# Optimization experiments

Measured on AMD Instinct MI355X. Metric: run time of the kernel, lower is better.

The kernel has to match this reference:

```python
import jax, jax.numpy as jnp
import numpy as np

Z_DIM = 16
N_EVAL = 1
MAX_LATENT_VARIANCE = 0.1


def _decoder(z, V1, c1, V2, c2, Vsig, csig):
    # z: (B, n) -> x_star: (B, D), sigma: (B,) per-sample positive scalar
    h = jnp.tanh(z @ V1 + c1)
    x_star = h @ V2 + c2
    sigma = jax.nn.softplus(h @ Vsig + csig)[:, 0] + 1e-3
    return x_star, sigma


def _encoder(x, W1, b1, W2, b2):
    h = jnp.tanh(x @ W1 + b1)
    return h @ W2 + b2


def _f_hess(z, x, dec):
    # faithful port of function_for_hessian: scalar per-sample energy
    D = x.shape[0]
    x_star, sigma = _decoder(z[None], *dec)
    d = (x[None] - x_star) / sigma[:, None]
    return (d * d).sum() / 2 + D * jnp.log(sigma).sum() + (z ** 2).sum() / 2


def setup_inputs() -> dict:
    key = jax.random.key(0)
    ks = jax.random.split(key, 8)
    B, D, H, n = 256, 3072, 2048, Z_DIM
    return {
        "x": jax.random.uniform(ks[0], (B, D), jnp.float32),
        "W1": jax.random.normal(ks[1], (D, H), jnp.float32) / np.sqrt(D).astype(np.float32),
        "b1": jnp.zeros((H,), jnp.float32),
        "W2": jax.random.normal(ks[2], (H, n), jnp.float32) / np.sqrt(H).astype(np.float32),
        "b2": jnp.zeros((n,), jnp.float32),
        "V1": jax.random.normal(ks[3], (n, H), jnp.float32) / np.sqrt(n).astype(np.float32),
        "c1": jnp.zeros((H,), jnp.float32),
        "V2": jax.random.normal(ks[4], (H, D), jnp.float32) / np.sqrt(H).astype(np.float32),
        "c2": jnp.zeros((D,), jnp.float32),
        "Vsig": jax.random.normal(ks[5], (H, 1), jnp.float32) / np.sqrt(H).astype(np.float32),
        "csig": jnp.zeros((1,), jnp.float32),
        "eps": jax.random.normal(ks[6], (N_EVAL, B, n), jnp.float32),
    }


def reference(x, W1, b1, W2, b2, V1, c1, V2, c2, Vsig, csig, eps):
    dec = (V1, c1, V2, c2, Vsig, csig)
    z_star = _encoder(x, W1, b1, W2, b2)            # (B, n)
    B, D = x.shape
    n = z_star.shape[1]
    n_eval = eps.shape[0]

    # per-sample Hessian of the energy wrt z (double autodiff through decoder)
    hess = jax.vmap(jax.hessian(_f_hess), in_axes=(0, 0, None))(z_star, x, dec)  # (B, n, n)

    eigvals = jnp.linalg.eigvalsh(hess)             # (B, n)
    delta = jnp.maximum(1.0 / MAX_LATENT_VARIANCE - eigvals.min(axis=1), 0.0)    # (B,)
    Prec = hess + jnp.eye(n, dtype=hess.dtype) * delta[:, None, None]
    eigvals = eigvals + delta[:, None]

    # upper Cholesky U with U^T U = Prec (matches torch cholesky(upper=True))
    U = jnp.swapaxes(jnp.linalg.cholesky(Prec), -1, -2)
    sol = jax.vmap(lambda e: jax.lax.linalg.triangular_solve(
        U, e[..., None], left_side=True, lower=False)[..., 0])(eps)  # (n_eval, B, n)
    z_sample = z_star[None] + sol

    recon, sigma = _decoder(z_sample.reshape(-1, n), *dec)           # (n_eval*B, D), (n_eval*B,)
    x_rep = jnp.tile(x, (n_eval, 1))
    recon_loss = (((recon - x_rep) / sigma[:, None]) ** 2).sum(axis=1) / 2
    recon_loss = recon_loss.reshape(n_eval, B).mean(axis=0)

    latent_energy = (z_star ** 2).sum(axis=1) / 2 + (1.0 / eigvals).sum(axis=1) / 2
    logdet_loss = jnp.log(eigvals).sum(axis=1) / 2
    sigma_loss = (D * jnp.log(sigma)).reshape(n_eval, B).mean(axis=0)

    neg_log_prob = (recon_loss + latent_energy + logdet_loss + sigma_loss) / D
    return neg_log_prob
```

## Files before the change

kernel.cpp:

```cpp
#include <hip/hip_runtime.h>
#include <math.h>

#define B_N 256
#define D_N 3072
#define H_N 2048

typedef __bf16 bf16x8 __attribute__((ext_vector_type(8)));
typedef float f32x4 __attribute__((ext_vector_type(4)));

__device__ __forceinline__ void async16(const void* g, void* l) {
  __builtin_amdgcn_global_load_lds(
      (const __attribute__((address_space(1))) unsigned int*)g,
      (__attribute__((address_space(3))) unsigned int*)l, 16, 0, 0);
}

template<int EPI>
__global__ __launch_bounds__(256) void gemm_nn(const float* __restrict__ A,
        const float* __restrict__ Bm, const float* __restrict__ bias,
        const float* __restrict__ X, float* __restrict__ C,
        int M, int N, int K) {
  __shared__ __align__(16) float As[16][64];
  __shared__ __align__(16) float Bs[16][68];
  int tid = threadIdx.x;
  int tx = tid & 15, ty = tid >> 4;
  int n0 = blockIdx.x * 64, m0 = blockIdx.y * 64;
  float acc[4][4] = {};
  int am = tid >> 2, akq = (tid & 3) * 4;
  int bn = tid & 63, bk0 = (tid >> 6) * 4;
  for (int k0 = 0; k0 < K; k0 += 16) {
    float4 a4 = *(const float4*)(A + (size_t)(m0 + am) * K + k0 + akq);
    As[akq + 0][am] = a4.x; As[akq + 1][am] = a4.y;
    As[akq + 2][am] = a4.z; As[akq + 3][am] = a4.w;
#pragma unroll
    for (int p = 0; p < 4; ++p) {
      int kk = bk0 + p;
      Bs[kk][bn] = Bm[(size_t)(k0 + kk) * N + n0 + bn];
    }
    __syncthreads();
#pragma unroll
    for (int kk = 0; kk < 16; ++kk) {
      float4 av = *(const float4*)&As[kk][ty * 4];
      float4 bv = *(const float4*)&Bs[kk][tx * 4];
      float a_[4] = {av.x, av.y, av.z, av.w};
      float b_[4] = {bv.x, bv.y, bv.z, bv.w};
#pragma unroll
      for (int i = 0; i < 4; ++i)
#pragma unroll
        for (int j = 0; j < 4; ++j)
          acc[i][j] = fmaf(a_[i], b_[j], acc[i][j]);
    }
    __syncthreads();
  }
#pragma unroll
  for (int i = 0; i < 4; ++i) {
    int m = m0 + ty * 4 + i;
#pragma unroll
    for (int j = 0; j < 4; ++j) {
      int n = n0 + tx * 4 + j;
      float v = acc[i][j];
      if (EPI == 0) {
        v = tanhf(v + bias[n]);
      } else {
        v = X[(size_t)m * N + n] - v - bias[n];
      }
      C[(size_t)m * N + n] = v;
    }
  }
}

__global__ __launch_bounds__(256) void gemm_nt(const float* __restrict__ A,
        const float* __restrict__ B2, float* __restrict__ C, int M, int N, int K) {
  __shared__ __align__(16) float As[16][64];
  __shared__ __align__(16) float Bs[16][68];
  int tid = threadIdx.x;
  int tx = tid & 15, ty = tid >> 4;
  int n0 = blockIdx.x * 64, m0 = blockIdx.y * 64;
  float acc[4][4] = {};
  int am = tid >> 2, akq = (tid & 3) * 4;
  for (int k0 = 0; k0 < K; k0 += 16) {
    float4 a4 = *(const float4*)(A + (size_t)(m0 + am) * K + k0 + akq);
    As[akq + 0][am] = a4.x; As[akq + 1][am] = a4.y;
    As[akq + 2][am] = a4.z; As[akq + 3][am] = a4.w;
    float4 b4 = *(const float4*)(B2 + (size_t)(n0 + am) * K + k0 + akq);
    Bs[akq + 0][am] = b4.x; Bs[akq + 1][am] = b4.y;
    Bs[akq + 2][am] = b4.z; Bs[akq + 3][am] = b4.w;
    __syncthreads();
#pragma unroll
    for (int kk = 0; kk < 16; ++kk) {
      float4 av = *(const float4*)&As[kk][ty * 4];
      float4 bv = *(const float4*)&Bs[kk][tx * 4];
      float a_[4] = {av.x, av.y, av.z, av.w};
      float b_[4] = {bv.x, bv.y, bv.z, bv.w};
#pragma unroll
      for (int i = 0; i < 4; ++i)
#pragma unroll
        for (int j = 0; j < 4; ++j)
          acc[i][j] = fmaf(a_[i], b_[j], acc[i][j]);
    }
    __syncthreads();
  }
#pragma unroll
  for (int i = 0; i < 4; ++i)
#pragma unroll
    for (int j = 0; j < 4; ++j)
      C[(size_t)(m0 + ty * 4 + i) * N + n0 + tx * 4 + j] = acc[i][j];
}

template<int EPI>
__global__ __launch_bounds__(256) void mfma_gemm(const float* __restrict__ A,
        const __bf16* __restrict__ Bt, const float* __restrict__ bias,
        const float* __restrict__ X, float* __restrict__ C,
        int M, int N, int K) {
  __shared__ __align__(16) __bf16 Aa[64][72];
  __shared__ __align__(16) __bf16 Bb[64][72];
  int tid = threadIdx.x;
  int lane = tid & 63, w = tid >> 6;
  int n0 = blockIdx.x * 64, m0 = blockIdx.y * 64;
  f32x4 acc[4] = {};
  int srow = tid >> 2, sk = (tid & 3) * 16;
  const float* arow_p = A + (size_t)(m0 + srow) * K;
  const __bf16* brow_p = Bt + (size_t)(n0 + srow) * K;
  int ar = lane & 15, aq = (lane >> 4) * 8;
  for (int k0 = 0; k0 < K; k0 += 64) {
    __bf16 tmp[16];
#pragma unroll
    for (int p = 0; p < 16; p += 4) {
      float4 a4 = *(const float4*)(arow_p + k0 + sk + p);
      tmp[p + 0] = (__bf16)a4.x; tmp[p + 1] = (__bf16)a4.y;
      tmp[p + 2] = (__bf16)a4.z; tmp[p + 3] = (__bf16)a4.w;
    }
    *(uint4*)&Aa[srow][sk] = *(uint4*)&tmp[0];
    *(uint4*)&Aa[srow][sk + 8] = *(uint4*)&tmp[8];
    *(uint4*)&Bb[srow][sk] = *(const uint4*)(brow_p + k0 + sk);
    *(uint4*)&Bb[srow][sk + 8] = *(const uint4*)(brow_p + k0 + sk + 8);
    __syncthreads();
#pragma unroll
    for (int kk = 0; kk < 64; kk += 32) {
      bf16x8 a = *(const bf16x8*)&Aa[w * 16 + ar][kk + aq];
#pragma unroll
      for (int cg = 0; cg < 4; ++cg) {
        bf16x8 bb = *(const bf16x8*)&Bb[cg * 16 + ar][kk + aq];
        acc[cg] = __builtin_amdgcn_mfma_f32_16x16x32_bf16(a, bb, acc[cg], 0, 0, 0);
      }
    }
    __syncthreads();
  }
  int crow = (lane >> 4) * 4;
#pragma unroll
  for (int cg = 0; cg < 4; ++cg) {
#pragma unroll
    for (int r = 0; r < 4; ++r) {
      int m = m0 + w * 16 + crow + r;
      int n = n0 + cg * 16 + ar;
      float v = acc[cg][r];
      if (EPI == 0) v = tanhf(v + bias[n]);
      else if (EPI == 1) v = X[(size_t)m * N + n] - v - bias[n];
      C[(size_t)m * N + n] = v;
    }
  }
}

__global__ __launch_bounds__(256) void gemm64_sk(const __bf16* __restrict__ A,
        const __bf16* __restrict__ Bt, float* __restrict__ P, int M, int N, int K) {
  __shared__ __align__(16) __bf16 Ab[64 * 64];
  __shared__ __align__(16) __bf16 Bb[64 * 64];
  int tid = threadIdx.x;
  int lane = tid & 63, w = tid >> 6;
  int n0 = blockIdx.x * 64, m0 = blockIdx.y * 64;
  int k0 = blockIdx.z * 512;
  int srow = lane >> 3;
  int schunk = (lane & 7) ^ (srow & 7);
  const char* gA[2];
  const char* gB[2];
#pragma unroll
  for (int i = 0; i < 2; ++i) {
    int r = 16 * w + 8 * i + srow;
    gA[i] = (const char*)(A + (size_t)(m0 + r) * K + k0) + schunk * 16;
    gB[i] = (const char*)(Bt + (size_t)(n0 + r) * K + k0) + schunk * 16;
  }
  f32x4 acc[4] = {};
  int ar = lane & 15, aq = (lane >> 4) * 8;
  int sw = ar & 7;
  for (int it = 0; it < 8; ++it) {
#pragma unroll
    for (int i = 0; i < 2; ++i) {
      async16(gA[i], (char*)Ab + (16 * w + 8 * i) * 128);
      async16(gB[i], (char*)Bb + (16 * w + 8 * i) * 128);
      gA[i] += 128;
      gB[i] += 128;
    }
    __syncthreads();
#pragma unroll
    for (int kk = 0; kk < 64; kk += 32) {
      int ch = (kk + aq) >> 3;
      int coff = (ch ^ sw) * 16;
      bf16x8 a = *(const bf16x8*)((char*)Ab + (16 * w + ar) * 128 + coff);
#pragma unroll
      for (int cg = 0; cg < 4; ++cg) {
        bf16x8 bb = *(const bf16x8*)((char*)Bb + (cg * 16 + ar) * 128 + coff);
        acc[cg] = __builtin_amdgcn_mfma_f32_16x16x32_bf16(a, bb, acc[cg], 0, 0, 0);
      }
    }
    __syncthreads();
  }
  int q = lane >> 4;
  float* Pz = P + (size_t)blockIdx.z * M * N;
#pragma unroll
  for (int cg = 0; cg < 4; ++cg)
#pragma unroll
    for (int r = 0; r < 4; ++r) {
      int m = m0 + 16 * w + q * 4 + r;
      int n = n0 + cg * 16 + ar;
      Pz[(size_t)m * N + n] = acc[cg][r];
    }
}

template<int EPI, int WBF>
__global__ __launch_bounds__(256) void reduce_epi(const float* __restrict__ P,
        const float* __restrict__ bias, const float* __restrict__ X,
        float* __restrict__ C, __bf16* __restrict__ Cbf, int M, int N, int S) {
  int idx = (blockIdx.x * 256 + threadIdx.x) * 4;
  size_t MN = (size_t)M * N;
  float4 s = *(const float4*)(P + idx);
  for (int z = 1; z < S; ++z) {
    float4 p = *(const float4*)(P + z * MN + idx);
    s.x += p.x; s.y += p.y; s.z += p.z; s.w += p.w;
  }
  int n = idx % N;
  float v[4] = {s.x, s.y, s.z, s.w};
  if (EPI == 0) {
#pragma unroll
    for (int j = 0; j < 4; ++j) v[j] = tanhf(v[j] + bias[n + j]);
  } else if (EPI == 1) {
    float4 xv = *(const float4*)(X + idx);
    float xa[4] = {xv.x, xv.y, xv.z, xv.w};
#pragma unroll
    for (int j = 0; j < 4; ++j) v[j] = xa[j] - v[j] - bias[n + j];
  }
  *(float4*)(C + idx) = make_float4(v[0], v[1], v[2], v[3]);
  if (WBF) {
    __bf16 t[4] = {(__bf16)v[0], (__bf16)v[1], (__bf16)v[2], (__bf16)v[3]};
    *(uint2*)(Cbf + idx) = *(uint2*)&t[0];
  }
}

__global__ __launch_bounds__(256) void build_J(const float* __restrict__ h,
        const float* __restrict__ V1, __bf16* __restrict__ J) {
  int row = blockIdx.x;
  int b = row >> 4, i = row & 15;
  int k = threadIdx.x * 8;
  const float* hp = h + (size_t)b * H_N + k;
  const float* vp = V1 + (size_t)i * H_N + k;
  float4 h0 = *(const float4*)hp, h1 = *(const float4*)(hp + 4);
  float4 v0 = *(const float4*)vp, v1 = *(const float4*)(vp + 4);
  __bf16 t[8];
  t[0] = (__bf16)((1.f - h0.x * h0.x) * v0.x);
  t[1] = (__bf16)((1.f - h0.y * h0.y) * v0.y);
  t[2] = (__bf16)((1.f - h0.z * h0.z) * v0.z);
  t[3] = (__bf16)((1.f - h0.w * h0.w) * v0.w);
  t[4] = (__bf16)((1.f - h1.x * h1.x) * v1.x);
  t[5] = (__bf16)((1.f - h1.y * h1.y) * v1.y);
  t[6] = (__bf16)((1.f - h1.z * h1.z) * v1.z);
  t[7] = (__bf16)((1.f - h1.w * h1.w) * v1.w);
  *(uint4*)(J + (size_t)row * H_N + k) = *(uint4*)&t[0];
}

__global__ __launch_bounds__(256) void gemm128_nt_bf16(
        const __bf16* __restrict__ A, const __bf16* __restrict__ B,
        __bf16* __restrict__ C, int M, int N, int K) {
  __shared__ __align__(16) __bf16 Ab[128 * 64];
  __shared__ __align__(16) __bf16 Bb[128 * 64];
  int tid = threadIdx.x;
  int lane = tid & 63, w = tid >> 6;
  int m0 = blockIdx.y * 128, n0 = blockIdx.x * 128;
  int wm = w & 1, wn = w >> 1;
// ... 23 lines not shown
    for (int kk = 0; kk < 64; kk += 32) {
      int ch = (kk + aq) >> 3;
      int coff = (ch ^ sw) * 16;
      bf16x8 af[4], bfr[4];
#pragma unroll
      for (int f = 0; f < 4; ++f) {
        int rowA = wm * 64 + f * 16 + ar;
        af[f] = *(const bf16x8*)((char*)Ab + rowA * 128 + coff);
        int rowB = wn * 64 + f * 16 + ar;
        bfr[f] = *(const bf16x8*)((char*)Bb + rowB * 128 + coff);
      }
#pragma unroll
      for (int i = 0; i < 4; ++i)
#pragma unroll
        for (int j = 0; j < 4; ++j)
          acc[i][j] = __builtin_amdgcn_mfma_f32_16x16x32_bf16(af[i], bfr[j],
                                                              acc[i][j], 0, 0, 0);
    }
    __syncthreads();
  }
  int q = lane >> 4;
#pragma unroll
  for (int i = 0; i < 4; ++i)
#pragma unroll
    for (int j = 0; j < 4; ++j)
#pragma unroll
      for (int r = 0; r < 4; ++r) {
        int m = m0 + wm * 64 + i * 16 + q * 4 + r;
        int n = n0 + wn * 64 + j * 16 + ar;
        C[(size_t)m * N + n] = (__bf16)acc[i][j][r];
      }
}

__global__ __launch_bounds__(256) void gram16(const __bf16* __restrict__ Mbf,
        const float* __restrict__ coef, float* __restrict__ Hm) {
  __shared__ float red[4][16][17];
  int b = blockIdx.x;
  int tid = threadIdx.x, lane = tid & 63, w = tid >> 6;
  int ar = lane & 15, q = lane >> 4;
  const __bf16* row = Mbf + (size_t)(b * 16 + ar) * D_N + w * (D_N / 4);
  f32x4 acc = {};
  for (int k = 0; k < D_N / 4; k += 32) {
    bf16x8 a = *(const bf16x8*)(row + k + q * 8);
    acc = __builtin_amdgcn_mfma_f32_16x16x32_bf16(a, a, acc, 0, 0, 0);
  }
#pragma unroll
  for (int r = 0; r < 4; ++r) red[w][q * 4 + r][ar] = acc[r];
  __syncthreads();
  int i = tid >> 4, j = tid & 15;
  float g = red[0][i][j] + red[1][i][j] + red[2][i][j] + red[3][i][j];
  Hm[(size_t)b * 256 + tid] += coef[b * 4] * g;
}

__global__ __launch_bounds__(256) void small_mfma3(const float* __restrict__ h,
        const float* __restrict__ t, const float* __restrict__ Vsig,
        const float* __restrict__ V1, const float* __restrict__ coef,
        float* __restrict__ Hm) {
  __shared__ float redT[4][16][17];
  __shared__ float redP[4][4][16];
  __shared__ float redQ[4][4][16];
  int b = blockIdx.x;
  int tid = threadIdx.x, lane = tid & 63, w = tid >> 6;
  int m = lane & 15, q = lane >> 4;
  float a1 = coef[b * 4 + 0], a2 = coef[b * 4 + 1];
  float beta = coef[b * 4 + 2], csp = coef[b * 4 + 3];
  const float* hb = h + (size_t)b * H_N;
  const float* tb = t + (size_t)b * H_N;
  const float* vr = V1 + (size_t)m * H_N;
  f32x4 accT = {};
  float pacc = 0.f, qacc = 0.f;
  for (int s = 0; s < 16; ++s) {
    int kb = w * 512 + s * 32 + q * 8;
    float hv[8], tv[8], sv[8], v1v[8];
    *(float4*)&hv[0] = *(const float4*)(hb + kb);
    *(float4*)&hv[4] = *(const float4*)(hb + kb + 4);
    *(float4*)&tv[0] = *(const float4*)(tb + kb);
    *(float4*)&tv[4] = *(const float4*)(tb + kb + 4);
    *(float4*)&sv[0] = *(const float4*)(Vsig + kb);
    *(float4*)&sv[4] = *(const float4*)(Vsig + kb + 4);
    *(float4*)&v1v[0] = *(const float4*)(vr + kb);
    *(float4*)&v1v[4] = *(const float4*)(vr + kb + 4);
    __bf16 ah[8], al[8], bh[8], bl[8];
#pragma unroll
    for (int j = 0; j < 8; ++j) {
      float hk = hv[j];
      float dk = 1.f - hk * hk;
      float g = fmaf(csp, sv[j], -a1 * tv[j]);
      float wk = -2.f * g * hk * dk;
      float av = wk * v1v[j];
      __bf16 avh = (__bf16)av;
      ah[j] = avh;
      al[j] = (__bf16)(av - (float)avh);
      __bf16 bvh = (__bf16)v1v[j];
      bh[j] = bvh;
      bl[j] = (__bf16)(v1v[j] - (float)bvh);
      pacc = fmaf(dk * tv[j], v1v[j], pacc);
      qacc = fmaf(dk * sv[j], v1v[j], qacc);
    }
    accT = __builtin_amdgcn_mfma_f32_16x16x32_bf16(*(bf16x8*)ah, *(bf16x8*)bh,
                                                   accT, 0, 0, 0);
    accT = __builtin_amdgcn_mfma_f32_16x16x32_bf16(*(bf16x8*)ah, *(bf16x8*)bl,
                                                   accT, 0, 0, 0);
    accT = __builtin_amdgcn_mfma_f32_16x16x32_bf16(*(bf16x8*)al, *(bf16x8*)bh,
                                                   accT, 0, 0, 0);
  }
#pragma unroll
  for (int r = 0; r < 4; ++r) redT[w][q * 4 + r][m] = accT[r];
  redP[w][q][m] = pacc;
  redQ[w][q][m] = qacc;
  __syncthreads();
  int i = tid >> 4, j = tid & 15;
  float T2 = redT[0][i][j] + redT[1][i][j] + redT[2][i][j] + redT[3][i][j];
  float pi_ = 0.f, qi_ = 0.f, pj_ = 0.f, qj_ = 0.f;
#pragma unroll
  for (int ww = 0; ww < 4; ++ww)
#pragma unroll
    for (int qq = 0; qq < 4; ++qq) {
      pi_ += redP[ww][qq][i]; qi_ += redQ[ww][qq][i];
      pj_ += redP[ww][qq][j]; qj_ += redQ[ww][qq][j];
    }
  float v = T2 + a2 * (pi_ * qj_ + qi_ * pj_) + beta * qi_ * qj_
          + ((i == j) ? 1.f : 0.f);
  Hm[(size_t)b * 256 + i * 16 + j] = v;
}

__global__ __launch_bounds__(256) void enc_z(const float* __restrict__ henc,
        const float* __restrict__ W2, const float* __restrict__ b2,
        float* __restrict__ zs) {
  __shared__ float red[16 * 256];
  int b = blockIdx.x, tid = threadIdx.x;
  float p[16] = {};
  for (int k = tid; k < H_N; k += 256) {
    float hv = henc[(size_t)b * H_N + k];
#pragma unroll
    for (int i = 0; i < 16; ++i) p[i] = fmaf(hv, W2[k * 16 + i], p[i]);
  }
#pragma unroll
  for (int i = 0; i < 16; ++i) red[i * 256 + tid] = p[i];
  __syncthreads();
  for (int off = 128; off > 0; off >>= 1) {
    if (tid < off)
#pragma unroll
      for (int i = 0; i < 16; ++i) red[i * 256 + tid] += red[i * 256 + tid + off];
    __syncthreads();
  }
  if (tid < 16) zs[b * 16 + tid] = red[tid * 256] + b2[tid];
}

__global__ __launch_bounds__(256) void dec_h(const float* __restrict__ z,
        const float* __restrict__ V1, const float* __restrict__ c1,
        float* __restrict__ h, __bf16* __restrict__ hb) {
  int b = blockIdx.y;
  int k = blockIdx.x * 256 + threadIdx.x;
  float acc = c1[k];
#pragma unroll
  for (int i = 0; i < 16; ++i) acc = fmaf(z[b * 16 + i], V1[i * H_N + k], acc);
  float v = tanhf(acc);
  h[(size_t)b * H_N + k] = v;
  if (hb) hb[(size_t)b * H_N + k] = (__bf16)v;
}

__global__ __launch_bounds__(256) void row_sigma(const float* __restrict__ h,
        const float* __restrict__ Vsig, const float* __restrict__ csig,
        float* __restrict__ sig, float* __restrict__ sp) {
  __shared__ float red[256];
  int b = blockIdx.x, tid = threadIdx.x;
  float s = 0.f;
  for (int k = tid; k < H_N; k += 256) s = fmaf(h[(size_t)b * H_N + k], Vsig[k], s);
  red[tid] = s; __syncthreads();
  for (int off = 128; off > 0; off >>= 1) {
    if (tid < off) red[tid] += red[tid + off];
    __syncthreads();
  }
  if (tid == 0) {
    float t = red[0] + csig[0];
    float spl = fmaxf(t, 0.f) + log1pf(expf(-fabsf(t)));
    sig[b] = spl + 1e-3f;
    sp[b] = 1.f / (1.f + expf(-t));
  }
}

__global__ __launch_bounds__(256) void row_sq(const float* __restrict__ r,
        float* __restrict__ S, int N) {
  __shared__ float red[256];
  int b = blockIdx.x, tid = threadIdx.x;
  float s = 0.f;
  for (int j = tid; j < N; j += 256) { float v = r[(size_t)b * N + j]; s = fmaf(v, v, s); }
  red[tid] = s; __syncthreads();
  for (int off = 128; off > 0; off >>= 1) {
    if (tid < off) red[tid] += red[tid + off];
    __syncthreads();
  }
// ... 60 lines not shown
  }
  if (tid >= 136 && tid < 152) pS[tid - 136] = accP;
  if (tid >= 152 && tid < 168) qS[tid - 152] = accQ;
  __syncthreads();
  if (tid < 136) {
    float v = accT + a2 * (pS[pi] * qS[pj] + qS[pi] * pS[pj]) + beta * qS[pi] * qS[pj];
    if (pi == pj) v += 1.f;
    Hm[(size_t)b * 256 + pi * 16 + pj] = v;
    Hm[(size_t)b * 256 + pj * 16 + pi] = v;
  }
}

__global__ __launch_bounds__(256) void conv_t_bf16(const float* __restrict__ src,
        __bf16* __restrict__ dst, int K, int N) {
  __shared__ float T[32][33];
  int n0 = blockIdx.x * 32, k0 = blockIdx.y * 32;
  int x = threadIdx.x & 31, y = threadIdx.x >> 5;
#pragma unroll
  for (int p = 0; p < 4; ++p)
    T[y + 8 * p][x] = src[(size_t)(k0 + y + 8 * p) * N + n0 + x];
  __syncthreads();
#pragma unroll
  for (int p = 0; p < 4; ++p)
    dst[(size_t)(n0 + y + 8 * p) * K + k0 + x] = (__bf16)T[x][y + 8 * p];
}

__global__ __launch_bounds__(256) void conv_bf16(const float* __restrict__ src,
        __bf16* __restrict__ dst, int n) {
  int i = (blockIdx.x * 256 + threadIdx.x) * 4;
  if (i < n) {
    float4 v = *(const float4*)(src + i);
    __bf16 t[4] = {(__bf16)v.x, (__bf16)v.y, (__bf16)v.z, (__bf16)v.w};
    *(uint2*)(dst + i) = *(uint2*)&t[0];
  }
}

__global__ __launch_bounds__(256) void fused_gram_mfma(const float* __restrict__ h,
        const float* __restrict__ V1, const __bf16* __restrict__ V2T,
        const float* __restrict__ coef, float* __restrict__ Hm) {
  __shared__ __align__(16) __bf16 Ja[64][72];
  __shared__ __align__(16) __bf16 Vb[64][72];
  __shared__ float Mf[64][68];
  int tid = threadIdx.x;
  int lane = tid & 63, w = tid >> 6;
  int j0 = blockIdx.x * 64;
  int b0 = blockIdx.y * 4;
  f32x4 acc[4] = {};
  int srow = tid >> 2;
  int sk = (tid & 3) * 16;
  int s_s = srow >> 4, s_i = srow & 15;
  const float* hrow = h + (size_t)(b0 + s_s) * H_N;
  const float* v1row = V1 + (size_t)s_i * H_N;
  const __bf16* v2row = V2T + (size_t)(j0 + srow) * H_N;
  int ar = lane & 15, aq = (lane >> 4) * 8;
  for (int k0 = 0; k0 < H_N; k0 += 64) {
    __bf16 tmp[16];
#pragma unroll
    for (int p = 0; p < 16; p += 4) {
      float4 h4 = *(const float4*)(hrow + k0 + sk + p);
      float4 v4 = *(const float4*)(v1row + k0 + sk + p);
      tmp[p + 0] = (__bf16)((1.f - h4.x * h4.x) * v4.x);
      tmp[p + 1] = (__bf16)((1.f - h4.y * h4.y) * v4.y);
      tmp[p + 2] = (__bf16)((1.f - h4.z * h4.z) * v4.z);
      tmp[p + 3] = (__bf16)((1.f - h4.w * h4.w) * v4.w);
    }
    *(uint4*)&Ja[srow][sk] = *(uint4*)&tmp[0];
    *(uint4*)&Ja[srow][sk + 8] = *(uint4*)&tmp[8];
    *(uint4*)&Vb[srow][sk] = *(const uint4*)(v2row + k0 + sk);
    *(uint4*)&Vb[srow][sk + 8] = *(const uint4*)(v2row + k0 + sk + 8);
    __syncthreads();
#pragma unroll
    for (int kk = 0; kk < 64; kk += 32) {
      bf16x8 a = *(const bf16x8*)&Ja[w * 16 + ar][kk + aq];
#pragma unroll
      for (int cg = 0; cg < 4; ++cg) {
        bf16x8 bb = *(const bf16x8*)&Vb[cg * 16 + ar][kk + aq];
        acc[cg] = __builtin_amdgcn_mfma_f32_16x16x32_bf16(a, bb, acc[cg], 0, 0, 0);
      }
    }
    __syncthreads();
  }
  int crow = (lane >> 4) * 4;
#pragma unroll
  for (int cg = 0; cg < 4; ++cg)
#pragma unroll
    for (int r = 0; r < 4; ++r)
      Mf[w * 16 + crow + r][cg * 16 + ar] = acc[cg][r];
  __syncthreads();
  for (int pp = tid; pp < 544; pp += 256) {
    int s = pp / 136, pr = pp % 136;
    int i = 0, p = pr;
    while (p >= 16 - i) { p -= 16 - i; ++i; }
    int jj = i + p;
    float sum = 0.f;
    for (int j = 0; j < 64; ++j)
      sum = fmaf(Mf[s * 16 + i][j], Mf[s * 16 + jj][j], sum);
    sum *= coef[(b0 + s) * 4 + 0];
    atomicAdd(&Hm[(size_t)(b0 + s) * 256 + i * 16 + jj], sum);
    if (i != jj) atomicAdd(&Hm[(size_t)(b0 + s) * 256 + jj * 16 + i], sum);
  }
}

__global__ __launch_bounds__(256) void eig_chol_lane(const float* __restrict__ Hm,
        const float* __restrict__ zs, const float* __restrict__ eps,
        float* __restrict__ zsamp, float* __restrict__ outpart) {
  int tid = threadIdx.x;
  int g = tid & 15;
  int b = blockIdx.x * 16 + (tid >> 4);
  const float* Ab = Hm + (size_t)b * 256;
  float a[16], orig[16];
#pragma unroll
  for (int r = 0; r < 16; ++r) { orig[r] = Ab[r * 16 + g]; a[r] = orig[r]; }
  float ev[15];
  float u[16], w[16];
#pragma unroll
  for (int k = 0; k < 14; ++k) {
    float x1 = __shfl(a[k + 1], k, 16);
    float xn2 = 0.f;
#pragma unroll
    for (int r = k + 2; r < 16; ++r) {
      u[r] = __shfl(a[r], k, 16);
      xn2 = fmaf(u[r], u[r], xn2);
    }
    float nrm = sqrtf(x1 * x1 + xn2);
    float alpha = (x1 >= 0.f) ? -nrm : nrm;
    float uk1 = x1 - alpha;
    u[k + 1] = uk1;
    float tau = 2.f / fmaxf(uk1 * uk1 + xn2, 1e-30f);
    float uown = (g == k + 1) ? uk1 : ((g > k + 1) ? a[k] : 0.f);
    float s = 0.f;
#pragma unroll
    for (int r = k + 1; r < 16; ++r) s = fmaf(a[r], u[r], s);
// ... 115 lines not shown
  const float* x    = (const float*)d_in[0];
  const float* W1   = (const float*)d_in[1];
  const float* b1   = (const float*)d_in[2];
  const float* W2   = (const float*)d_in[3];
  const float* b2   = (const float*)d_in[4];
  const float* V1   = (const float*)d_in[5];
  const float* c1   = (const float*)d_in[6];
  const float* V2   = (const float*)d_in[7];
  const float* c2   = (const float*)d_in[8];
  const float* Vsig = (const float*)d_in[9];
  const float* csig = (const float*)d_in[10];
  const float* eps  = (const float*)d_in[11];

  float* ws = (float*)d_ws;
  float* henc  = ws + 0;
  float* h     = ws + 524288;
  float* rbuf  = ws + 1048576;
  float* tbuf  = ws + 1835008;
  float* zs    = ws + 2359296;
  float* zsamp = ws + 2363392;
  float* sig   = ws + 2367488;
  float* sp    = sig + 256;
  float* Sv    = sig + 512;
  float* sig2  = sig + 768;
  float* sp2   = sig + 1024;
  float* SS2   = sig + 1280;
  float* outp  = sig + 1536;
  float* coef  = ws + 2371584;
  float* Hm    = ws + 2372608;
  __bf16* V2T  = (__bf16*)(ws + 2438144);
  __bf16* W1T  = (__bf16*)(ws + 5583872);
  __bf16* V2bf = (__bf16*)(ws + 8729600);
  __bf16* Jbf  = (__bf16*)(ws + 11875328);
  float*  Pb   = ws + 11875328;
  __bf16* Mbf  = (__bf16*)(ws + 16069632);
  __bf16* x_bf = (__bf16*)(ws + 22361088);
  __bf16* h_bf = (__bf16*)(ws + 22754304);
  __bf16* r_bf = (__bf16*)(ws + 23016448);
  size_t need_mfma = (size_t)2438144 * 4 + (size_t)D_N * H_N * 2;
  size_t need_full = (size_t)11875328 * 4;
  size_t need_big  = (size_t)22361088 * 4;
  size_t need_sk   = (size_t)23409664 * 4;
  bool use_mfma = ws_size >= need_mfma;
  bool use_full = ws_size >= need_full;
  bool use_big  = ws_size >= need_big;
  bool use_sk   = ws_size >= need_sk;

  if (use_mfma)
    conv_t_bf16<<<dim3(D_N / 32, H_N / 32), 256, 0, stream>>>(V2, V2T, H_N, D_N);
  if (use_full) {
    conv_t_bf16<<<dim3(H_N / 32, D_N / 32), 256, 0, stream>>>(W1, W1T, D_N, H_N);
    conv_bf16<<<(H_N * D_N) / 1024, 256, 0, stream>>>(V2, V2bf, H_N * D_N);
  }
  if (use_sk)
    conv_bf16<<<(B_N * D_N) / 1024, 256, 0, stream>>>(x, x_bf, B_N * D_N);

  if (use_sk) {
    gemm64_sk<<<dim3(H_N / 64, B_N / 64, 6), 256, 0, stream>>>(x_bf, W1T, Pb,
                                                               B_N, H_N, D_N);
    reduce_epi<0, 0><<<(B_N * H_N) / 1024, 256, 0, stream>>>(Pb, b1, nullptr,
                                                             henc, nullptr,
                                                             B_N, H_N, 6);
  } else if (use_full) {
    mfma_gemm<0><<<dim3(H_N / 64, B_N / 64), 256, 0, stream>>>(x, W1T, b1, nullptr,
                                                               henc, B_N, H_N, D_N);
  } else {
    gemm_nn<0><<<dim3(H_N / 64, B_N / 64), 256, 0, stream>>>(x, W1, b1, nullptr,
                                                             henc, B_N, H_N, D_N);
  }
  enc_z<<<B_N, 256, 0, stream>>>(henc, W2, b2, zs);
  dec_h<<<dim3(H_N / 256, B_N), 256, 0, stream>>>(zs, V1, c1, h,
                                                  use_sk ? h_bf : nullptr);
  if (use_sk) {
    gemm64_sk<<<dim3(D_N / 64, B_N / 64, 4), 256, 0, stream>>>(h_bf, V2T, Pb,
                                                               B_N, D_N, H_N);
    reduce_epi<1, 1><<<(B_N * D_N) / 1024, 256, 0, stream>>>(Pb, c2, x,
                                                             rbuf, r_bf,
                                                             B_N, D_N, 4);
  } else if (use_full) {
    mfma_gemm<1><<<dim3(D_N / 64, B_N / 64), 256, 0, stream>>>(h, V2T, c2, x, rbuf,
                                                               B_N, D_N, H_N);
  } else {
    gemm_nn<1><<<dim3(D_N / 64, B_N / 64), 256, 0, stream>>>(h, V2, c2, x, rbuf,
                                                             B_N, D_N, H_N);
  }
  row_sigma<<<B_N, 256, 0, stream>>>(h, Vsig, csig, sig, sp);
  row_sq<<<B_N, 256, 0, stream>>>(rbuf, Sv, D_N);
  coefk<<<1, 256, 0, stream>>>(Sv, sig, sp, coef);
  if (use_sk) {
    gemm64_sk<<<dim3(H_N / 64, B_N / 64, 6), 256, 0, stream>>>(r_bf, V2bf, Pb,
                                                               B_N, H_N, D_N);
    reduce_epi<2, 0><<<(B_N * H_N) / 1024, 256, 0, stream>>>(Pb, nullptr, nullptr,
                                                             tbuf, nullptr,
                                                             B_N, H_N, 6);
  } else if (use_full) {
    mfma_gemm<2><<<dim3(H_N / 64, B_N / 64), 256, 0, stream>>>(rbuf, V2bf, nullptr,
                                                               nullptr, tbuf,
                                                               B_N, H_N, D_N);
  } else {
    gemm_nt<<<dim3(H_N / 64, B_N / 64), 256, 0, stream>>>(rbuf, V2, tbuf,
                                                          B_N, H_N, D_N);
  }
  if (use_sk)
    small_mfma3<<<B_N, 256, 0, stream>>>(h, tbuf, Vsig, V1, coef, Hm);
  else
    small_terms<<<B_N, 256, 0, stream>>>(h, tbuf, Vsig, V1, coef, Hm);
  if (use_big) {
    build_J<<<B_N * 16, 256, 0, stream>>>(h, V1, Jbf);
    gemm128_nt_bf16<<<dim3(D_N / 128, (B_N * 16) / 128), 256, 0, stream>>>(
        Jbf, V2T, Mbf, B_N * 16, D_N, H_N);
    gram16<<<B_N, 256, 0, stream>>>(Mbf, coef, Hm);
  } else if (use_mfma) {
    fused_gram_mfma<<<dim3(D_N / 64, B_N / 4), 256, 0, stream>>>(h, V1, V2T, coef, Hm);
  }
  eig_chol_lane<<<B_N / 16, 256, 0, stream>>>(Hm, zs, eps, zsamp, outp);
  dec_h<<<dim3(H_N / 256, B_N), 256, 0, stream>>>(zsamp, V1, c1, henc,
                                                  use_sk ? h_bf : nullptr);
  row_sigma<<<B_N, 256, 0, stream>>>(henc, Vsig, csig, sig2, sp2);
  if (use_sk) {
    gemm64_sk<<<dim3(D_N / 64, B_N / 64, 4), 256, 0, stream>>>(h_bf, V2T, Pb,
                                                               B_N, D_N, H_N);
    reduce_epi<1, 0><<<(B_N * D_N) / 1024, 256, 0, stream>>>(Pb, c2, x,
                                                             rbuf, nullptr,
                                                             B_N, D_N, 4);
  } else if (use_full) {
    mfma_gemm<1><<<dim3(D_N / 64, B_N / 64), 256, 0, stream>>>(henc, V2T, c2, x, rbuf,
                                                               B_N, D_N, H_N);
  } else {
    gemm_nn<1><<<dim3(D_N / 64, B_N / 64), 256, 0, stream>>>(henc, V2, c2, x, rbuf,
                                                             B_N, D_N, H_N);
  }
  row_sq<<<B_N, 256, 0, stream>>>(rbuf, SS2, D_N);
  final_k<<<1, 256, 0, stream>>>(SS2, sig2, outp, (float*)d_out);
}
```

Measured before the change: 317.0 us.

## Fuse decoder, sigma, J-build and row-square reductions into fewer kernels on fast path

On the split-K path the decoder hidden layer, sigma softplus and Jacobian construction now run in one dec_sig kernel. Row squared-norm sums are folded into the split-K reduce epilogue with atomics, replacing the separate row_sq kernels and the fp32 residual writes. The Gram term and the small Hessian terms are merged into one hess_assemble kernel. The aim is fewer launches and less global traffic. In exchange, atomic accumulation needs a zeroing kernel, the fp32 fallback paths are simplified, and dead kernels are removed.

```diff
diff --git a/kernel.cpp b/kernel.cpp
--- a/kernel.cpp
+++ b/kernel.cpp
@@ -12,6 +12,11 @@
   __builtin_amdgcn_global_load_lds(
       (const __attribute__((address_space(1))) unsigned int*)g,
       (__attribute__((address_space(3))) unsigned int*)l, 16, 0, 0);
+}
+
+__global__ void zero_k(float* __restrict__ a, float* __restrict__ b) {
+  a[threadIdx.x] = 0.f;
+  b[threadIdx.x] = 0.f;
 }
 
 template<int EPI>
@@ -68,98 +73,6 @@
   }
 }
 
-__global__ __launch_bounds__(256) void gemm_nt(const float* __restrict__ A,
-        const float* __restrict__ B2, float* __restrict__ C, int M, int N, int K) {
-  __shared__ __align__(16) float As[16][64];
-  __shared__ __align__(16) float Bs[16][68];
-  int tid = threadIdx.x;
-  int tx = tid & 15, ty = tid >> 4;
-  int n0 = blockIdx.x * 64, m0 = blockIdx.y * 64;
-  float acc[4][4] = {};
-  int am = tid >> 2, akq = (tid & 3) * 4;
-  for (int k0 = 0; k0 < K; k0 += 16) {
-    float4 a4 = *(const float4*)(A + (size_t)(m0 + am) * K + k0 + akq);
-    As[akq + 0][am] = a4.x; As[akq + 1][am] = a4.y;
-    As[akq + 2][am] = a4.z; As[akq + 3][am] = a4.w;
-    float4 b4 = *(const float4*)(B2 + (size_t)(n0 + am) * K + k0 + akq);
-    Bs[akq + 0][am] = b4.x; Bs[akq + 1][am] = b4.y;
-    Bs[akq + 2][am] = b4.z; Bs[akq + 3][am] = b4.w;
-    __syncthreads();
-#pragma unroll
-    for (int kk = 0; kk < 16; ++kk) {
-      float4 av = *(const float4*)&As[kk][ty * 4];
-      float4 bv = *(const float4*)&Bs[kk][tx * 4];
-      float a_[4] = {av.x, av.y, av.z, av.w};
-      float b_[4] = {bv.x, bv.y, bv.z, bv.w};
-#pragma unroll
-      for (int i = 0; i < 4; ++i)
-#pragma unroll
-        for (int j = 0; j < 4; ++j)
-          acc[i][j] = fmaf(a_[i], b_[j], acc[i][j]);
-    }
-    __syncthreads();
-  }
-#pragma unroll
-  for (int i = 0; i < 4; ++i)
-#pragma unroll
-    for (int j = 0; j < 4; ++j)
-      C[(size_t)(m0 + ty * 4 + i) * N + n0 + tx * 4 + j] = acc[i][j];
-}
-
-template<int EPI>
-__global__ __launch_bounds__(256) void mfma_gemm(const float* __restrict__ A,
-        const __bf16* __restrict__ Bt, const float* __restrict__ bias,
-        const float* __restrict__ X, float* __restrict__ C,
-        int M, int N, int K) {
-  __shared__ __align__(16) __bf16 Aa[64][72];
-  __shared__ __align__(16) __bf16 Bb[64][72];
-  int tid = threadIdx.x;
-  int lane = tid & 63, w = tid >> 6;
-  int n0 = blockIdx.x * 64, m0 = blockIdx.y * 64;
-  f32x4 acc[4] = {};
-  int srow = tid >> 2, sk = (tid & 3) * 16;
-  const float* arow_p = A + (size_t)(m0 + srow) * K;
-  const __bf16* brow_p = Bt + (size_t)(n0 + srow) * K;
-  int ar = lane & 15, aq = (lane >> 4) * 8;
-  for (int k0 = 0; k0 < K; k0 += 64) {
-    __bf16 tmp[16];
-#pragma unroll
-    for (int p = 0; p < 16; p += 4) {
-      float4 a4 = *(const float4*)(arow_p + k0 + sk + p);
-      tmp[p + 0] = (__bf16)a4.x; tmp[p + 1] = (__bf16)a4.y;
-      tmp[p + 2] = (__bf16)a4.z; tmp[p + 3] = (__bf16)a4.w;
-    }
-    *(uint4*)&Aa[srow][sk] = *(uint4*)&tmp[0];
-    *(uint4*)&Aa[srow][sk + 8] = *(uint4*)&tmp[8];
-    *(uint4*)&Bb[srow][sk] = *(const uint4*)(brow_p + k0 + sk);
-    *(uint4*)&Bb[srow][sk + 8] = *(const uint4*)(brow_p + k0 + sk + 8);
-    __syncthreads();
-#pragma unroll
-    for (int kk = 0; kk < 64; kk += 32) {
-      bf16x8 a = *(const bf16x8*)&Aa[w * 16 + ar][kk + aq];
-#pragma unroll
-      for (int cg = 0; cg < 4; ++cg) {
-        bf16x8 bb = *(const bf16x8*)&Bb[cg * 16 + ar][kk + aq];
-        acc[cg] = __builtin_amdgcn_mfma_f32_16x16x32_bf16(a, bb, acc[cg], 0, 0, 0);
-      }
-    }
-    __syncthreads();
-  }
-  int crow = (lane >> 4) * 4;
-#pragma unroll
-  for (int cg = 0; cg < 4; ++cg) {
-#pragma unroll
-    for (int r = 0; r < 4; ++r) {
-      int m = m0 + w * 16 + crow + r;
-      int n = n0 + cg * 16 + ar;
-      float v = acc[cg][r];
-      if (EPI == 0) v = tanhf(v + bias[n]);
-      else if (EPI == 1) v = X[(size_t)m * N + n] - v - bias[n];
-      C[(size_t)m * N + n] = v;
-    }
-  }
-}
-
 __global__ __launch_bounds__(256) void gemm64_sk(const __bf16* __restrict__ A,
         const __bf16* __restrict__ Bt, float* __restrict__ P, int M, int N, int K) {
   __shared__ __align__(16) __bf16 Ab[64 * 64];
@@ -215,10 +128,12 @@
     }
 }
 
-template<int EPI, int WBF>
+template<int EPI, int WBF, int SQ, int WC>
 __global__ __launch_bounds__(256) void reduce_epi(const float* __restrict__ P,
         const float* __restrict__ bias, const float* __restrict__ X,
-        float* __restrict__ C, __bf16* __restrict__ Cbf, int M, int N, int S) {
+        float* __restrict__ C, __bf16* __restrict__ Cbf,
+        float* __restrict__ Ssum, int M, int N, int S) {
+  __shared__ float red[256];
   int idx = (blockIdx.x * 256 + threadIdx.x) * 4;
   size_t MN = (size_t)M * N;
   float4 s = *(const float4*)(P + idx);
@@ -237,10 +152,65 @@
 #pragma unroll
     for (int j = 0; j < 4; ++j) v[j] = xa[j] - v[j] - bias[n + j];
   }
-  *(float4*)(C + idx) = make_float4(v[0], v[1], v[2], v[3]);
+  if (WC) *(float4*)(C + idx) = make_float4(v[0], v[1], v[2], v[3]);
   if (WBF) {
     __bf16 t[4] = {(__bf16)v[0], (__bf16)v[1], (__bf16)v[2], (__bf16)v[3]};
     *(uint2*)(Cbf + idx) = *(uint2*)&t[0];
+  }
+  if (SQ) {
+    float sq = v[0] * v[0] + v[1] * v[1] + v[2] * v[2] + v[3] * v[3];
+    red[threadIdx.x] = sq;
+    __syncthreads();
+    for (int off = 128; off > 0; off >>= 1) {
+      if (threadIdx.x < off) red[threadIdx.x] += red[threadIdx.x + off];
+      __syncthreads();
+    }
+    if (threadIdx.x == 0) {
+      int row = (blockIdx.x * 1024) / N;
+      atomicAdd(&Ssum[row], red[0]);
+    }
+  }
+}
+
+template<int WJ>
+__global__ __launch_bounds__(256) void dec_sig(const float* __restrict__ z,
+        const float* __restrict__ V1, const float* __restrict__ c1,
+        const float* __restrict__ Vsig, const float* __restrict__ csig,
+        float* __restrict__ h, __bf16* __restrict__ hb, __bf16* __restrict__ J,
+        float* __restrict__ sig, float* __restrict__ sp) {
+  __shared__ float red[256];
+  int b = blockIdx.x, tid = threadIdx.x;
+  float zloc[16];
+#pragma unroll
+  for (int i = 0; i < 16; ++i) zloc[i] = z[b * 16 + i];
+  float partial = 0.f;
+  for (int j = 0; j < 8; ++j) {
+    int k = j * 256 + tid;
+    float acc = c1[k];
+#pragma unroll
+    for (int i = 0; i < 16; ++i) acc = fmaf(zloc[i], V1[i * H_N + k], acc);
+    float v = tanhf(acc);
+    if (h) h[(size_t)b * H_N + k] = v;
+    hb[(size_t)b * H_N + k] = (__bf16)v;
+    partial = fmaf(v, Vsig[k], partial);
+    if (WJ) {
+      float d = 1.f - v * v;
+#pragma unroll
+      for (int i = 0; i < 16; ++i)
+        J[(size_t)(b * 16 + i) * H_N + k] = (__bf16)(d * V1[i * H_N + k]);
+    }
+  }
+  red[tid] = partial;
+  __syncthreads();
+  for (int off = 128; off > 0; off >>= 1) {
+    if (tid < off) red[tid] += red[tid + off];
+    __syncthreads();
+  }
+  if (tid == 0) {
+    float t = red[0] + csig[0];
+    float spl = fmaxf(t, 0.f) + log1pf(expf(-fabsf(t)));
+    sig[b] = spl + 1e-3f;
+    sp[b] = 1.f / (1.f + expf(-t));
   }
 }
 
@@ -330,31 +300,12 @@
       }
 }
 
-__global__ __launch_bounds__(256) void gram16(const __bf16* __restrict__ Mbf,
+__global__ __launch_bounds__(256) void hess_assemble(const float* __restrict__ h,
+        const float* __restrict__ t, const float* __restrict__ Vsig,
+        const float* __restrict__ V1, const __bf16* __restrict__ Mbf,
         const float* __restrict__ coef, float* __restrict__ Hm) {
-  __shared__ float red[4][16][17];
-  int b = blockIdx.x;
-  int tid = threadIdx.x, lane = tid & 63, w = tid >> 6;
-  int ar = lane & 15, q = lane >> 4;
-  const __bf16* row = Mbf + (size_t)(b * 16 + ar) * D_N + w * (D_N / 4);
-  f32x4 acc = {};
-  for (int k = 0; k < D_N / 4; k += 32) {
-    bf16x8 a = *(const bf16x8*)(row + k + q * 8);
-    acc = __builtin_amdgcn_mfma_f32_16x16x32_bf16(a, a, acc, 0, 0, 0);
-  }
-#pragma unroll
-  for (int r = 0; r < 4; ++r) red[w][q * 4 + r][ar] = acc[r];
-  __syncthreads();
-  int i = tid >> 4, j = tid & 15;
-  float g = red[0][i][j] + red[1][i][j] + red[2][i][j] + red[3][i][j];
-  Hm[(size_t)b * 256 + tid] += coef[b * 4] * g;
-}
-
-__global__ __launch_bounds__(256) void small_mfma3(const float* __restrict__ h,
-        const float* __restrict__ t, const float* __restrict__ Vsig,
-        const float* __restrict__ V1, const float* __restrict__ coef,
-        float* __restrict__ Hm) {
   __shared__ float redT[4][16][17];
+  __shared__ float redG[4][16][17];
   __shared__ float redP[4][4][16];
   __shared__ float redQ[4][4][16];
   int b = blockIdx.x;
@@ -402,13 +353,23 @@
     accT = __builtin_amdgcn_mfma_f32_16x16x32_bf16(*(bf16x8*)al, *(bf16x8*)bh,
                                                    accT, 0, 0, 0);
   }
-#pragma unroll
-  for (int r = 0; r < 4; ++r) redT[w][q * 4 + r][m] = accT[r];
+  const __bf16* grow = Mbf + (size_t)(b * 16 + m) * D_N + w * (D_N / 4);
+  f32x4 accG = {};
+  for (int k = 0; k < D_N / 4; k += 32) {
+    bf16x8 a = *(const bf16x8*)(grow + k + q * 8);
+    accG = __builtin_amdgcn_mfma_f32_16x16x32_bf16(a, a, accG, 0, 0, 0);
+  }
+#pragma unroll
+  for (int r = 0; r < 4; ++r) {
+    redT[w][q * 4 + r][m] = accT[r];
+    redG[w][q * 4 + r][m] = accG[r];
+  }
   redP[w][q][m] = pacc;
   redQ[w][q][m] = qacc;
   __syncthreads();
   int i = tid >> 4, j = tid & 15;
   float T2 = redT[0][i][j] + redT[1][i][j] + redT[2][i][j] + redT[3][i][j];
+  float G = redG[0][i][j] + redG[1][i][j] + redG[2][i][j] + redG[3][i][j];
   float pi_ = 0.f, qi_ = 0.f, pj_ = 0.f, qj_ = 0.f;
 #pragma unroll
   for (int ww = 0; ww < 4; ++ww)
@@ -418,8 +379,28 @@
       pj_ += redP[ww][qq][j]; qj_ += redQ[ww][qq][j];
     }
   float v = T2 + a2 * (pi_ * qj_ + qi_ * pj_) + beta * qi_ * qj_
-          + ((i == j) ? 1.f : 0.f);
+          + ((i == j) ? 1.f : 0.f) + a1 * G;
   Hm[(size_t)b * 256 + i * 16 + j] = v;
+}
+
+__global__ __launch_bounds__(256) void gram16(const __bf16* __restrict__ Mbf,
+        const float* __restrict__ coef, float* __restrict__ Hm) {
+  __shared__ float red[4][16][17];
+  int b = blockIdx.x;
+  int tid = threadIdx.x, lane = tid & 63, w = tid >> 6;
+  int ar = lane & 15, q = lane >> 4;
+  const __bf16* row = Mbf + (size_t)(b * 16 + ar) * D_N + w * (D_N / 4);
+  f32x4 acc = {};
+  for (int k = 0; k < D_N / 4; k += 32) {
+    bf16x8 a = *(const bf16x8*)(row + k + q * 8);
+    acc = __builtin_amdgcn_mfma_f32_16x16x32_bf16(a, a, acc, 0, 0, 0);
+  }
+#pragma unroll
+  for (int r = 0; r < 4; ++r) red[w][q * 4 + r][ar] = acc[r];
+  __syncthreads();
+  int i = tid >> 4, j = tid & 15;
+  float g = red[0][i][j] + red[1][i][j] + red[2][i][j] + red[3][i][j];
+  Hm[(size_t)b * 256 + tid] += coef[b * 4] * g;
 }
 
 __global__ __launch_bounds__(256) void enc_z(const float* __restrict__ henc,
@@ -447,15 +428,13 @@
 
 __global__ __launch_bounds__(256) void dec_h(const float* __restrict__ z,
         const float* __restrict__ V1, const float* __restrict__ c1,
-        float* __restrict__ h, __bf16* __restrict__ hb) {
+        float* __restrict__ h) {
   int b = blockIdx.y;
   int k = blockIdx.x * 256 + threadIdx.x;
   float acc = c1[k];
 #pragma unroll
   for (int i = 0; i < 16; ++i) acc = fmaf(z[b * 16 + i], V1[i * H_N + k], acc);
-  float v = tanhf(acc);
-  h[(size_t)b * H_N + k] = v;
-  if (hb) hb[(size_t)b * H_N + k] = (__bf16)v;
+  h[(size_t)b * H_N + k] = tanhf(acc);
 }
 
 __global__ __launch_bounds__(256) void row_sigma(const float* __restrict__ h,
@@ -582,72 +561,6 @@
     float4 v = *(const float4*)(src + i);
     __bf16 t[4] = {(__bf16)v.x, (__bf16)v.y, (__bf16)v.z, (__bf16)v.w};
     *(uint2*)(dst + i) = *(uint2*)&t[0];
-  }
-}
-
-__global__ __launch_bounds__(256) void fused_gram_mfma(const float* __restrict__ h,
-        const float* __restrict__ V1, const __bf16* __restrict__ V2T,
-        const float* __restrict__ coef, float* __restrict__ Hm) {
-  __shared__ __align__(16) __bf16 Ja[64][72];
-  __shared__ __align__(16) __bf16 Vb[64][72];
-  __shared__ float Mf[64][68];
-  int tid = threadIdx.x;
-  int lane = tid & 63, w = tid >> 6;
-  int j0 = blockIdx.x * 64;
-  int b0 = blockIdx.y * 4;
-  f32x4 acc[4] = {};
-  int srow = tid >> 2;
-  int sk = (tid & 3) * 16;
-  int s_s = srow >> 4, s_i = srow & 15;
-  const float* hrow = h + (size_t)(b0 + s_s) * H_N;
-  const float* v1row = V1 + (size_t)s_i * H_N;
-  const __bf16* v2row = V2T + (size_t)(j0 + srow) * H_N;
-  int ar = lane & 15, aq = (lane >> 4) * 8;
-  for (int k0 = 0; k0 < H_N; k0 += 64) {
-    __bf16 tmp[16];
-#pragma unroll
-    for (int p = 0; p < 16; p += 4) {
-      float4 h4 = *(const float4*)(hrow + k0 + sk + p);
-      float4 v4 = *(const float4*)(v1row + k0 + sk + p);
-      tmp[p + 0] = (__bf16)((1.f - h4.x * h4.x) * v4.x);
-      tmp[p + 1] = (__bf16)((1.f - h4.y * h4.y) * v4.y);
-      tmp[p + 2] = (__bf16)((1.f - h4.z * h4.z) * v4.z);
-      tmp[p + 3] = (__bf16)((1.f - h4.w * h4.w) * v4.w);
-    }
-    *(uint4*)&Ja[srow][sk] = *(uint4*)&tmp[0];
-    *(uint4*)&Ja[srow][sk + 8] = *(uint4*)&tmp[8];
-    *(uint4*)&Vb[srow][sk] = *(const uint4*)(v2row + k0 + sk);
-    *(uint4*)&Vb[srow][sk + 8] = *(const uint4*)(v2row + k0 + sk + 8);
-    __syncthreads();
-#pragma unroll
-    for (int kk = 0; kk < 64; kk += 32) {
-      bf16x8 a = *(const bf16x8*)&Ja[w * 16 + ar][kk + aq];
-#pragma unroll
-      for (int cg = 0; cg < 4; ++cg) {
-        bf16x8 bb = *(const bf16x8*)&Vb[cg * 16 + ar][kk + aq];
-        acc[cg] = __builtin_amdgcn_mfma_f32_16x16x32_bf16(a, bb, acc[cg], 0, 0, 0);
-      }
-    }
-    __syncthreads();
-  }
-  int crow = (lane >> 4) * 4;
-#pragma unroll
-  for (int cg = 0; cg < 4; ++cg)
-#pragma unroll
-    for (int r = 0; r < 4; ++r)
-      Mf[w * 16 + crow + r][cg * 16 + ar] = acc[cg][r];
-  __syncthreads();
-  for (int pp = tid; pp < 544; pp += 256) {
-    int s = pp / 136, pr = pp % 136;
-    int i = 0, p = pr;
-    while (p >= 16 - i) { p -= 16 - i; ++i; }
-    int jj = i + p;
-    float sum = 0.f;
-    for (int j = 0; j < 64; ++j)
-      sum = fmaf(Mf[s * 16 + i][j], Mf[s * 16 + jj][j], sum);
-    sum *= coef[(b0 + s) * 4 + 0];
-    atomicAdd(&Hm[(size_t)(b0 + s) * 256 + i * 16 + jj], sum);
-    if (i != jj) atomicAdd(&Hm[(size_t)(b0 + s) * 256 + jj * 16 + i], sum);
   }
 }
 
@@ -829,104 +742,77 @@
   __bf16* W1T  = (__bf16*)(ws + 5583872);
   __bf16* V2bf = (__bf16*)(ws + 8729600);
   __bf16* Jbf  = (__bf16*)(ws + 11875328);
-  float*  Pb   = ws + 11875328;
   __bf16* Mbf  = (__bf16*)(ws + 16069632);
+  float*  Pb   = ws + 16069632;
   __bf16* x_bf = (__bf16*)(ws + 22361088);
   __bf16* h_bf = (__bf16*)(ws + 22754304);
   __bf16* r_bf = (__bf16*)(ws + 23016448);
-  size_t need_mfma = (size_t)2438144 * 4 + (size_t)D_N * H_N * 2;
   size_t need_full = (size_t)11875328 * 4;
-  size_t need_big  = (size_t)22361088 * 4;
   size_t need_sk   = (size_t)23409664 * 4;
-  bool use_mfma = ws_size >= need_mfma;
   bool use_full = ws_size >= need_full;
-  bool use_big  = ws_size >= need_big;
   bool use_sk   = ws_size >= need_sk;
 
-  if (use_mfma)
+  if (use_sk) {
+    zero_k<<<1, 256, 0, stream>>>(Sv, SS2);
     conv_t_bf16<<<dim3(D_N / 32, H_N / 32), 256, 0, stream>>>(V2, V2T, H_N, D_N);
-  if (use_full) {
     conv_t_bf16<<<dim3(H_N / 32, D_N / 32), 256, 0, stream>>>(W1, W1T, D_N, H_N);
     conv_bf16<<<(H_N * D_N) / 1024, 256, 0, stream>>>(V2, V2bf, H_N * D_N);
-  }
-  if (use_sk)
     conv_bf16<<<(B_N * D_N) / 1024, 256, 0, stream>>>(x, x_bf, B_N * D_N);
-
-  if (use_sk) {
     gemm64_sk<<<dim3(H_N / 64, B_N / 64, 6), 256, 0, stream>>>(x_bf, W1T, Pb,
                                                                B_N, H_N, D_N);
-    reduce_epi<0, 0><<<(B_N * H_N) / 1024, 256, 0, stream>>>(Pb, b1, nullptr,
-                                                             henc, nullptr,
-                                                             B_N, H_N, 6);
-  } else if (use_full) {
-    mfma_gemm<0><<<dim3(H_N / 64, B_N / 64), 256, 0, stream>>>(x, W1T, b1, nullptr,
-                                                               henc, B_N, H_N, D_N);
-  } else {
-    gemm_nn<0><<<dim3(H_N / 64, B_N / 64), 256, 0, stream>>>(x, W1, b1, nullptr,
-                                                             henc, B_N, H_N, D_N);
-  }
-  enc_z<<<B_N, 256, 0, stream>>>(henc, W2, b2, zs);
-  dec_h<<<dim3(H_N / 256, B_N), 256, 0, stream>>>(zs, V1, c1, h,
-                                                  use_sk ? h_bf : nullptr);
-  if (use_sk) {
+    reduce_epi<0, 0, 0, 1><<<(B_N * H_N) / 1024, 256, 0, stream>>>(
+        Pb, b1, nullptr, henc, nullptr, nullptr, B_N, H_N, 6);
+    enc_z<<<B_N, 256, 0, stream>>>(henc, W2, b2, zs);
+    dec_sig<1><<<B_N, 256, 0, stream>>>(zs, V1, c1, Vsig, csig, h, h_bf, Jbf,
+                                        sig, sp);
     gemm64_sk<<<dim3(D_N / 64, B_N / 64, 4), 256, 0, stream>>>(h_bf, V2T, Pb,
                                                                B_N, D_N, H_N);
-    reduce_epi<1, 1><<<(B_N * D_N) / 1024, 256, 0, stream>>>(Pb, c2, x,
-                                                             rbuf, r_bf,
-                                                             B_N, D_N, 4);
-  } else if (use_full) {
-    mfma_gemm<1><<<dim3(D_N / 64, B_N / 64), 256, 0, stream>>>(h, V2T, c2, x, rbuf,
+    reduce_epi<1, 1, 1, 0><<<(B_N * D_N) / 1024, 256, 0, stream>>>(
+        Pb, c2, x, nullptr, r_bf, Sv, B_N, D_N, 4);
+    coefk<<<1, 256, 0, stream>>>(Sv, sig, sp, coef);
+    gemm64_sk<<<dim3(H_N / 64, B_N / 64, 6), 256, 0, stream>>>(r_bf, V2bf, Pb,
+                                                               B_N, H_N, D_N);
+    reduce_epi<2, 0, 0, 1><<<(B_N * H_N) / 1024, 256, 0, stream>>>(
+        Pb, nullptr, nullptr, tbuf, nullptr, nullptr, B_N, H_N, 6);
+    gemm128_nt_bf16<<<dim3(D_N / 128, (B_N * 16) / 128), 256, 0, stream>>>(
+        Jbf, V2T, Mbf, B_N * 16, D_N, H_N);
+    hess_assemble<<<B_N, 256, 0, stream>>>(h, tbuf, Vsig, V1, Mbf, coef, Hm);
+    eig_chol_lane<<<B_N / 16, 256, 0, stream>>>(Hm, zs, eps, zsamp, outp);
+    dec_sig<0><<<B_N, 256, 0, stream>>>(zsamp, V1, c1, Vsig, csig, nullptr,
+                                        h_bf, nullptr, sig2, sp2);
+    gemm64_sk<<<dim3(D_N / 64, B_N / 64, 4), 256, 0, stream>>>(h_bf, V2T, Pb,
                                                                B_N, D_N, H_N);
-  } else {
-    gemm_nn<1><<<dim3(D_N / 64, B_N / 64), 256, 0, stream>>>(h, V2, c2, x, rbuf,
-                                                             B_N, D_N, H_N);
-  }
+    reduce_epi<1, 0, 1, 0><<<(B_N * D_N) / 1024, 256, 0, stream>>>(
+        Pb, c2, x, nullptr, nullptr, SS2, B_N, D_N, 4);
+    final_k<<<1, 256, 0, stream>>>(SS2, sig2, outp, (float*)d_out);
+    return;
+  }
+
+  if (use_full)
+    conv_t_bf16<<<dim3(D_N / 32, H_N / 32), 256, 0, stream>>>(V2, V2T, H_N, D_N);
+  gemm_nn<0><<<dim3(H_N / 64, B_N / 64), 256, 0, stream>>>(x, W1, b1, nullptr,
+                                                           henc, B_N, H_N, D_N);
+  enc_z<<<B_N, 256, 0, stream>>>(henc, W2, b2, zs);
+  dec_h<<<dim3(H_N / 256, B_N), 256, 0, stream>>>(zs, V1, c1, h);
+  gemm_nn<1><<<dim3(D_N / 64, B_N / 64), 256, 0, stream>>>(h, V2, c2, x, rbuf,
+                                                           B_N, D_N, H_N);
   row_sigma<<<B_N, 256, 0, stream>>>(h, Vsig, csig, sig, sp);
   row_sq<<<B_N, 256, 0, stream>>>(rbuf, Sv, D_N);
   coefk<<<1, 256, 0, stream>>>(Sv, sig, sp, coef);
-  if (use_sk) {
-    gemm64_sk<<<dim3(H_N / 64, B_N / 64, 6), 256, 0, stream>>>(r_bf, V2bf, Pb,
-                                                               B_N, H_N, D_N);
-    reduce_epi<2, 0><<<(B_N * H_N) / 1024, 256, 0, stream>>>(Pb, nullptr, nullptr,
-                                                             tbuf, nullptr,
-                                                             B_N, H_N, 6);
-  } else if (use_full) {
-    mfma_gemm<2><<<dim3(H_N / 64, B_N / 64), 256, 0, stream>>>(rbuf, V2bf, nullptr,
-                                                               nullptr, tbuf,
-                                                               B_N, H_N, D_N);
-  } else {
-    gemm_nt<<<dim3(H_N / 64, B_N / 64), 256, 0, stream>>>(rbuf, V2, tbuf,
-                                                          B_N, H_N, D_N);
-  }
-  if (use_sk)
-    small_mfma3<<<B_N, 256, 0, stream>>>(h, tbuf, Vsig, V1, coef, Hm);
-  else
-    small_terms<<<B_N, 256, 0, stream>>>(h, tbuf, Vsig, V1, coef, Hm);
-  if (use_big) {
+  {
+  }
+  small_terms<<<B_N, 256, 0, stream>>>(h, tbuf, Vsig, V1, coef, Hm);
+  if (use_full) {
     build_J<<<B_N * 16, 256, 0, stream>>>(h, V1, Jbf);
     gemm128_nt_bf16<<<dim3(D_N / 128, (B_N * 16) / 128), 256, 0, stream>>>(
         Jbf, V2T, Mbf, B_N * 16, D_N, H_N);
     gram16<<<B_N, 256, 0, stream>>>(Mbf, coef, Hm);
-  } else if (use_mfma) {
-    fused_gram_mfma<<<dim3(D_N / 64, B_N / 4), 256, 0, stream>>>(h, V1, V2T, coef, Hm);
   }
   eig_chol_lane<<<B_N / 16, 256, 0, stream>>>(Hm, zs, eps, zsamp, outp);
-  dec_h<<<dim3(H_N / 256, B_N), 256, 0, stream>>>(zsamp, V1, c1, henc,
-                                                  use_sk ? h_bf : nullptr);
+  dec_h<<<dim3(H_N / 256, B_N), 256, 0, stream>>>(zsamp, V1, c1, henc);
   row_sigma<<<B_N, 256, 0, stream>>>(henc, Vsig, csig, sig2, sp2);
-  if (use_sk) {
-    gemm64_sk<<<dim3(D_N / 64, B_N / 64, 4), 256, 0, stream>>>(h_bf, V2T, Pb,
-                                                               B_N, D_N, H_N);
-    reduce_epi<1, 0><<<(B_N * D_N) / 1024, 256, 0, stream>>>(Pb, c2, x,
-                                                             rbuf, nullptr,
-                                                             B_N, D_N, 4);
-  } else if (use_full) {
-    mfma_gemm<1><<<dim3(D_N / 64, B_N / 64), 256, 0, stream>>>(henc, V2T, c2, x, rbuf,
-                                                               B_N, D_N, H_N);
-  } else {
-    gemm_nn<1><<<dim3(D_N / 64, B_N / 64), 256, 0, stream>>>(henc, V2, c2, x, rbuf,
-                                                             B_N, D_N, H_N);
-  }
+  gemm_nn<1><<<dim3(D_N / 64, B_N / 64), 256, 0, stream>>>(henc, V2, c2, x, rbuf,
+                                                           B_N, D_N, H_N);
   row_sq<<<B_N, 256, 0, stream>>>(rbuf, SS2, D_N);
   final_k<<<1, 256, 0, stream>>>(SS2, sig2, outp, (float*)d_out);
 }
```

After: 309.4 us. 1.02x faster.
